# Performance work log

Measured on AMD Instinct MI355X. Metric: run time of the kernel, lower is better.

## Reference

```python
import jax, jax.numpy as jnp
import numpy as np

B, S, D, UNITS = 4, 512, 256, 128
NEG = -1e9


def setup_inputs() -> dict:
    key = jax.random.key(0)
    k1, k2, k3, k4 = jax.random.split(key, 4)
    values = jax.random.normal(k1, (B, S, D), dtype=jnp.float32)
    Wq = jax.random.normal(k2, (D, UNITS), dtype=jnp.float32) * (1.0 / np.sqrt(D))
    Wv = jax.random.normal(k3, (D, UNITS), dtype=jnp.float32) * (1.0 / np.sqrt(D))
    Vw = jax.random.normal(k4, (UNITS,), dtype=jnp.float32) * (1.0 / np.sqrt(UNITS))
    return {"values": values, "Wq": Wq, "Wv": Wv, "Vw": Vw}


def reference(values, Wq, Wv, Vw):
    # values: [B, S, D]
    query = values @ Wq            # [B, S, U]
    value = values @ Wv            # [B, S, U]
    # additive (Bahdanau) score: V . tanh(q_i + v_j) -> [B, S, S]
    feat = jnp.tanh(query[:, :, None, :] + value[:, None, :, :])  # [B,S,S,U]
    score = jnp.einsum('biju,u->bij', feat, Vw)
    seq_len = values.shape[1]
    causal = jnp.tril(jnp.ones((seq_len, seq_len), dtype=jnp.float32))  # lower-tri = visible
    score = score + (1.0 - causal)[None, :, :] * jnp.asarray(NEG, score.dtype)
    attn = jax.nn.softmax(score, axis=-1)          # [B, S, S]
    context = jnp.matmul(attn, values)             # [B, S, D]
    return context
```

## Files before the change

kernel.cpp:

```cpp
#include <hip/hip_runtime.h>
#include <hip/hip_fp16.h>

#define SEQ 512
#define DIM 256
#define UN  128
#define BSZ 2048
#define CSC 2.8853900817779268f

struct h8 { __half2 a, b, c, d; };

__global__ __launch_bounds__(256) void proj_kernel(
    const float* __restrict__ values, const float* __restrict__ Wq,
    const float* __restrict__ Wv, float* __restrict__ Qc, float* __restrict__ Vc,
    __half* __restrict__ Vf16) {
  __shared__ float vsm[4 * DIM];
  const int t = threadIdx.x;
  const int r0 = blockIdx.x * 4;
  {
    const int row = t >> 6, c4 = (t & 63) * 4;
    const float4 v = *(const float4*)(values + (r0 + row) * DIM + c4);
    *(float4*)&vsm[row * DIM + c4] = v;
    __half2* vf = (__half2*)(Vf16 + (r0 + row) * DIM + c4);
    vf[0] = __floats2half2_rn(v.x, v.y);
    vf[1] = __floats2half2_rn(v.z, v.w);
  }
  __syncthreads();
  const int half = t >> 7, u = t & 127;
  const float* __restrict__ W = half ? Wv : Wq;
  float acc[4] = {0.f, 0.f, 0.f, 0.f};
  for (int d = 0; d < DIM; d += 4) {
    const float w0 = W[(d + 0) * UN + u], w1 = W[(d + 1) * UN + u];
    const float w2 = W[(d + 2) * UN + u], w3 = W[(d + 3) * UN + u];
#pragma unroll
    for (int k = 0; k < 4; ++k) {
      const float4 v = *(const float4*)&vsm[k * DIM + d];
      acc[k] = fmaf(v.x, w0, acc[k]);
      acc[k] = fmaf(v.y, w1, acc[k]);
      acc[k] = fmaf(v.z, w2, acc[k]);
      acc[k] = fmaf(v.w, w3, acc[k]);
    }
  }
  if (!half) {
#pragma unroll
    for (int k = 0; k < 4; ++k) Qc[(r0 + k) * UN + u] = acc[k] * CSC;
  } else {
    const float4 o = make_float4(acc[0] * CSC, acc[1] * CSC, acc[2] * CSC, acc[3] * CSC);
    *(float4*)(Vc + u * BSZ + r0) = o;
  }
}

__global__ __launch_bounds__(256, 4) void attn_kernel(
    const __half* __restrict__ Vf16, const float* __restrict__ Qc,
    const float* __restrict__ Vc, const float* __restrict__ Vw,
    float* __restrict__ out) {
  __shared__ float sc[2 * SEQ];
  __shared__ float scp[2 * SEQ];
  __shared__ float part[8 * DIM];
  __shared__ float invs[2];

  const int t = threadIdx.x;
  const int b = blockIdx.x >> 8, p = blockIdx.x & 255;
  const int bS = b * SEQ;
  const int i = p;
  const int ihi = SEQ - 1 - p;
  const int jhi = ihi;

  const float* __restrict__ qlo = Qc + (bS + i) * UN;
  const float* __restrict__ qhi = Qc + (bS + ihi) * UN;

  {
    const int qd = t & 127;
    const int u0 = (t >> 7) << 6;
    const int jb = qd << 2;
    float* __restrict__ so = (t >> 7) ? scp : sc;
    const float* __restrict__ vq = Vc + bS + jb;
    if ((t & 64) == 0) {
      float h0=0.f,h1=0.f,h2=0.f,h3=0.f,l0=0.f,l1=0.f,l2=0.f,l3=0.f;
#pragma unroll 2
      for (int u = u0; u < u0 + 64; ++u) {
        const float4 vc = *(const float4*)(vq + (size_t)u * BSZ);
        const float qh = qhi[u], ql = qlo[u], w = Vw[u];
        h0 = fmaf(w, __builtin_amdgcn_rcpf(__builtin_amdgcn_exp2f(qh + vc.x) + 1.f), h0);
        h1 = fmaf(w, __builtin_amdgcn_rcpf(__builtin_amdgcn_exp2f(qh + vc.y) + 1.f), h1);
        h2 = fmaf(w, __builtin_amdgcn_rcpf(__builtin_amdgcn_exp2f(qh + vc.z) + 1.f), h2);
        h3 = fmaf(w, __builtin_amdgcn_rcpf(__builtin_amdgcn_exp2f(qh + vc.w) + 1.f), h3);
        l0 = fmaf(w, __builtin_amdgcn_rcpf(__builtin_amdgcn_exp2f(ql + vc.x) + 1.f), l0);
        l1 = fmaf(w, __builtin_amdgcn_rcpf(__builtin_amdgcn_exp2f(ql + vc.y) + 1.f), l1);
        l2 = fmaf(w, __builtin_amdgcn_rcpf(__builtin_amdgcn_exp2f(ql + vc.z) + 1.f), l2);
        l3 = fmaf(w, __builtin_amdgcn_rcpf(__builtin_amdgcn_exp2f(ql + vc.w) + 1.f), l3);
      }
      *(float4*)&so[SEQ + jb] = make_float4(h0, h1, h2, h3);
      *(float4*)&so[jb]       = make_float4(l0, l1, l2, l3);
    } else if (jb <= jhi) {
      float h0=0.f,h1=0.f,h2=0.f,h3=0.f;
#pragma unroll 4
      for (int u = u0; u < u0 + 64; ++u) {
        const float4 vc = *(const float4*)(vq + (size_t)u * BSZ);
        const float qh = qhi[u], w = Vw[u];
        h0 = fmaf(w, __builtin_amdgcn_rcpf(__builtin_amdgcn_exp2f(qh + vc.x) + 1.f), h0);
        h1 = fmaf(w, __builtin_amdgcn_rcpf(__builtin_amdgcn_exp2f(qh + vc.y) + 1.f), h1);
        h2 = fmaf(w, __builtin_amdgcn_rcpf(__builtin_amdgcn_exp2f(qh + vc.z) + 1.f), h2);
        h3 = fmaf(w, __builtin_amdgcn_rcpf(__builtin_amdgcn_exp2f(qh + vc.w) + 1.f), h3);
      }
      *(float4*)&so[SEQ + jb] = make_float4(h0, h1, h2, h3);
    }
  }
  __syncthreads();

  {
    const int w = t >> 6, l = t & 63;
    if (w < 2) {
      const int jmax = (w == 0) ? i : jhi;
      float* __restrict__ r0p = sc + w * SEQ;
      const float* __restrict__ r1p = scp + w * SEQ;
      float m = 1e30f;
      for (int j = l; j <= jmax; j += 64) m = fminf(m, r0p[j] + r1p[j]);
#pragma unroll
      for (int o = 32; o; o >>= 1) m = fminf(m, __shfl_xor(m, o));
      float sum = 0.f;
      for (int j = l; j <= jmax; j += 64) {
        const float pr = __builtin_amdgcn_exp2f((m - (r0p[j] + r1p[j])) * CSC);
        r0p[j] = pr;
        sum += pr;
      }
#pragma unroll
      for (int o = 32; o; o >>= 1) sum += __shfl_xor(sum, o);
      if (l == 0) invs[w] = __builtin_amdgcn_rcpf(sum);
    }
  }
  __syncthreads();

  {
    const int g = t >> 6, l = t & 63;
    const int jo = l >> 5, d8 = (l & 31) << 3;
    float alo[8], ahi[8];
#pragma unroll
    for (int k = 0; k < 8; ++k) { alo[k] = 0.f; ahi[k] = 0.f; }
    int j = 2 * g + jo;
    for (; j <= i; j += 8) {
      const float plo = sc[j], phi = sc[SEQ + j];
      const h8 v = *(const h8*)(Vf16 + (size_t)(bS + j) * DIM + d8);
      const float2 f0 = __half22float2(v.a), f1 = __half22float2(v.b);
      const float2 f2 = __half22float2(v.c), f3 = __half22float2(v.d);
      alo[0] = fmaf(plo, f0.x, alo[0]); alo[1] = fmaf(plo, f0.y, alo[1]);
      alo[2] = fmaf(plo, f1.x, alo[2]); alo[3] = fmaf(plo, f1.y, alo[3]);
      alo[4] = fmaf(plo, f2.x, alo[4]); alo[5] = fmaf(plo, f2.y, alo[5]);
      alo[6] = fmaf(plo, f3.x, alo[6]); alo[7] = fmaf(plo, f3.y, alo[7]);
      ahi[0] = fmaf(phi, f0.x, ahi[0]); ahi[1] = fmaf(phi, f0.y, ahi[1]);
      ahi[2] = fmaf(phi, f1.x, ahi[2]); ahi[3] = fmaf(phi, f1.y, ahi[3]);
      ahi[4] = fmaf(phi, f2.x, ahi[4]); ahi[5] = fmaf(phi, f2.y, ahi[5]);
      ahi[6] = fmaf(phi, f3.x, ahi[6]); ahi[7] = fmaf(phi, f3.y, ahi[7]);
    }
    for (; j <= jhi; j += 8) {
      const float phi = sc[SEQ + j];
      const h8 v = *(const h8*)(Vf16 + (size_t)(bS + j) * DIM + d8);
      const float2 f0 = __half22float2(v.a), f1 = __half22float2(v.b);
      const float2 f2 = __half22float2(v.c), f3 = __half22float2(v.d);
      ahi[0] = fmaf(phi, f0.x, ahi[0]); ahi[1] = fmaf(phi, f0.y, ahi[1]);
      ahi[2] = fmaf(phi, f1.x, ahi[2]); ahi[3] = fmaf(phi, f1.y, ahi[3]);
      ahi[4] = fmaf(phi, f2.x, ahi[4]); ahi[5] = fmaf(phi, f2.y, ahi[5]);
      ahi[6] = fmaf(phi, f3.x, ahi[6]); ahi[7] = fmaf(phi, f3.y, ahi[7]);
    }
#pragma unroll
    for (int k = 0; k < 8; ++k) {
      alo[k] += __shfl_xor(alo[k], 32);
      ahi[k] += __shfl_xor(ahi[k], 32);
    }
    if (jo == 0) {
      float* __restrict__ plo_ = &part[(g * 2 + 0) * DIM + d8];
      float* __restrict__ phi_ = &part[(g * 2 + 1) * DIM + d8];
      *(float4*)(plo_ + 0) = make_float4(alo[0], alo[1], alo[2], alo[3]);
      *(float4*)(plo_ + 4) = make_float4(alo[4], alo[5], alo[6], alo[7]);
      *(float4*)(phi_ + 0) = make_float4(ahi[0], ahi[1], ahi[2], ahi[3]);
      *(float4*)(phi_ + 4) = make_float4(ahi[4], ahi[5], ahi[6], ahi[7]);
    }
  }
  __syncthreads();

  {
    const float olo = (part[0 * DIM + t] + part[2 * DIM + t] +
                       part[4 * DIM + t] + part[6 * DIM + t]) * invs[0];
    const float ohi = (part[1 * DIM + t] + part[3 * DIM + t] +
                       part[5 * DIM + t] + part[7 * DIM + t]) * invs[1];
    out[(bS + i) * DIM + t] = olo;
    out[(bS + ihi) * DIM + t] = ohi;
  }
}

extern "C" void kernel_launch(void* const* d_in, const int* in_sizes, int n_in,
                              void* d_out, int out_size, void* d_ws, size_t ws_size,
                              hipStream_t stream) {
  const float* values = (const float*)d_in[0];
  const float* Wq     = (const float*)d_in[1];
  const float* Wv     = (const float*)d_in[2];
  const float* Vw     = (const float*)d_in[3];
  float* out = (float*)d_out;
  float* Qc   = (float*)d_ws;
  float* Vc   = Qc + (size_t)BSZ * UN;
  __half* Vf16 = (__half*)(Vc + (size_t)BSZ * UN);
  proj_kernel<<<dim3(BSZ / 4), 256, 0, stream>>>(values, Wq, Wv, Qc, Vc, Vf16);
  attn_kernel<<<dim3(4 * 256), 256, 0, stream>>>(Vf16, Qc, Vc, Vw, out);
}
```

Before: 118.1 us.

## Factor exp2 out of score inner loop and store value exponentials as bf16

Uses exp2(q+v)=exp2(q)*exp2(v) to precompute exponentials of the scaled query and value projections in the projection kernel. The score loop then needs only an fma and a reciprocal per element instead of an exp plus a reciprocal. The value exponentials are stored in bf16 to halve their read traffic. The score and context loops also software-prefetch the next row, at the cost of precision and overflow risk when exp2 of large projections is taken separately.

```diff
diff --git a/kernel.cpp b/kernel.cpp
--- a/kernel.cpp
+++ b/kernel.cpp
@@ -9,10 +9,19 @@
 
 struct h8 { __half2 a, b, c, d; };
 
+static __device__ __forceinline__ unsigned short f2bf(float x) {
+  unsigned u = __float_as_uint(x);
+  u += 0x7FFF + ((u >> 16) & 1);
+  return (unsigned short)(u >> 16);
+}
+static __device__ __forceinline__ float bf2f(unsigned short s) {
+  return __uint_as_float((unsigned)s << 16);
+}
+
 __global__ __launch_bounds__(256) void proj_kernel(
     const float* __restrict__ values, const float* __restrict__ Wq,
-    const float* __restrict__ Wv, float* __restrict__ Qc, float* __restrict__ Vc,
-    __half* __restrict__ Vf16) {
+    const float* __restrict__ Wv, float* __restrict__ Eq,
+    unsigned short* __restrict__ Ev, __half* __restrict__ Vf16) {
   __shared__ float vsm[4 * DIM];
   const int t = threadIdx.x;
   const int r0 = blockIdx.x * 4;
@@ -42,16 +51,21 @@
   }
   if (!half) {
 #pragma unroll
-    for (int k = 0; k < 4; ++k) Qc[(r0 + k) * UN + u] = acc[k] * CSC;
+    for (int k = 0; k < 4; ++k)
+      Eq[(r0 + k) * UN + u] = __builtin_amdgcn_exp2f(acc[k] * CSC);
   } else {
-    const float4 o = make_float4(acc[0] * CSC, acc[1] * CSC, acc[2] * CSC, acc[3] * CSC);
-    *(float4*)(Vc + u * BSZ + r0) = o;
+    ushort4 o;
+    o.x = f2bf(__builtin_amdgcn_exp2f(acc[0] * CSC));
+    o.y = f2bf(__builtin_amdgcn_exp2f(acc[1] * CSC));
+    o.z = f2bf(__builtin_amdgcn_exp2f(acc[2] * CSC));
+    o.w = f2bf(__builtin_amdgcn_exp2f(acc[3] * CSC));
+    *(ushort4*)(Ev + (size_t)u * BSZ + r0) = o;
   }
 }
 
 __global__ __launch_bounds__(256, 4) void attn_kernel(
-    const __half* __restrict__ Vf16, const float* __restrict__ Qc,
-    const float* __restrict__ Vc, const float* __restrict__ Vw,
+    const __half* __restrict__ Vf16, const float* __restrict__ Eq,
+    const unsigned short* __restrict__ Ev, const float* __restrict__ Vw,
     float* __restrict__ out) {
   __shared__ float sc[2 * SEQ];
   __shared__ float scp[2 * SEQ];
@@ -65,42 +79,46 @@
   const int ihi = SEQ - 1 - p;
   const int jhi = ihi;
 
-  const float* __restrict__ qlo = Qc + (bS + i) * UN;
-  const float* __restrict__ qhi = Qc + (bS + ihi) * UN;
-
-  {
-    const int qd = t & 127;
+  const float* __restrict__ eql = Eq + (bS + i) * UN;
+  const float* __restrict__ eqh = Eq + (bS + ihi) * UN;
+
+  {
+    const int qd = t & 127, jb = qd << 2;
     const int u0 = (t >> 7) << 6;
-    const int jb = qd << 2;
     float* __restrict__ so = (t >> 7) ? scp : sc;
-    const float* __restrict__ vq = Vc + bS + jb;
+    const unsigned short* __restrict__ evp = Ev + (size_t)u0 * BSZ + bS + jb;
     if ((t & 64) == 0) {
       float h0=0.f,h1=0.f,h2=0.f,h3=0.f,l0=0.f,l1=0.f,l2=0.f,l3=0.f;
-#pragma unroll 2
-      for (int u = u0; u < u0 + 64; ++u) {
-        const float4 vc = *(const float4*)(vq + (size_t)u * BSZ);
-        const float qh = qhi[u], ql = qlo[u], w = Vw[u];
-        h0 = fmaf(w, __builtin_amdgcn_rcpf(__builtin_amdgcn_exp2f(qh + vc.x) + 1.f), h0);
-        h1 = fmaf(w, __builtin_amdgcn_rcpf(__builtin_amdgcn_exp2f(qh + vc.y) + 1.f), h1);
-        h2 = fmaf(w, __builtin_amdgcn_rcpf(__builtin_amdgcn_exp2f(qh + vc.z) + 1.f), h2);
-        h3 = fmaf(w, __builtin_amdgcn_rcpf(__builtin_amdgcn_exp2f(qh + vc.w) + 1.f), h3);
-        l0 = fmaf(w, __builtin_amdgcn_rcpf(__builtin_amdgcn_exp2f(ql + vc.x) + 1.f), l0);
-        l1 = fmaf(w, __builtin_amdgcn_rcpf(__builtin_amdgcn_exp2f(ql + vc.y) + 1.f), l1);
-        l2 = fmaf(w, __builtin_amdgcn_rcpf(__builtin_amdgcn_exp2f(ql + vc.z) + 1.f), l2);
-        l3 = fmaf(w, __builtin_amdgcn_rcpf(__builtin_amdgcn_exp2f(ql + vc.w) + 1.f), l3);
+      ushort4 ec = *(const ushort4*)evp;
+#pragma unroll 4
+      for (int k = 0; k < 64; ++k) {
+        const ushort4 en = *(const ushort4*)(evp + (size_t)(k + 1) * BSZ);
+        const float qh = eqh[u0 + k], ql = eql[u0 + k], w = Vw[u0 + k];
+        const float e0 = bf2f(ec.x), e1 = bf2f(ec.y), e2 = bf2f(ec.z), e3 = bf2f(ec.w);
+        h0 = fmaf(w, __builtin_amdgcn_rcpf(fmaf(qh, e0, 1.f)), h0);
+        h1 = fmaf(w, __builtin_amdgcn_rcpf(fmaf(qh, e1, 1.f)), h1);
+        h2 = fmaf(w, __builtin_amdgcn_rcpf(fmaf(qh, e2, 1.f)), h2);
+        h3 = fmaf(w, __builtin_amdgcn_rcpf(fmaf(qh, e3, 1.f)), h3);
+        l0 = fmaf(w, __builtin_amdgcn_rcpf(fmaf(ql, e0, 1.f)), l0);
+        l1 = fmaf(w, __builtin_amdgcn_rcpf(fmaf(ql, e1, 1.f)), l1);
+        l2 = fmaf(w, __builtin_amdgcn_rcpf(fmaf(ql, e2, 1.f)), l2);
+        l3 = fmaf(w, __builtin_amdgcn_rcpf(fmaf(ql, e3, 1.f)), l3);
+        ec = en;
       }
       *(float4*)&so[SEQ + jb] = make_float4(h0, h1, h2, h3);
       *(float4*)&so[jb]       = make_float4(l0, l1, l2, l3);
     } else if (jb <= jhi) {
       float h0=0.f,h1=0.f,h2=0.f,h3=0.f;
+      ushort4 ec = *(const ushort4*)evp;
 #pragma unroll 4
-      for (int u = u0; u < u0 + 64; ++u) {
-        const float4 vc = *(const float4*)(vq + (size_t)u * BSZ);
-        const float qh = qhi[u], w = Vw[u];
-        h0 = fmaf(w, __builtin_amdgcn_rcpf(__builtin_amdgcn_exp2f(qh + vc.x) + 1.f), h0);
-        h1 = fmaf(w, __builtin_amdgcn_rcpf(__builtin_amdgcn_exp2f(qh + vc.y) + 1.f), h1);
-        h2 = fmaf(w, __builtin_amdgcn_rcpf(__builtin_amdgcn_exp2f(qh + vc.z) + 1.f), h2);
-        h3 = fmaf(w, __builtin_amdgcn_rcpf(__builtin_amdgcn_exp2f(qh + vc.w) + 1.f), h3);
+      for (int k = 0; k < 64; ++k) {
+        const ushort4 en = *(const ushort4*)(evp + (size_t)(k + 1) * BSZ);
+        const float qh = eqh[u0 + k], w = Vw[u0 + k];
+        h0 = fmaf(w, __builtin_amdgcn_rcpf(fmaf(qh, bf2f(ec.x), 1.f)), h0);
+        h1 = fmaf(w, __builtin_amdgcn_rcpf(fmaf(qh, bf2f(ec.y), 1.f)), h1);
+        h2 = fmaf(w, __builtin_amdgcn_rcpf(fmaf(qh, bf2f(ec.z), 1.f)), h2);
+        h3 = fmaf(w, __builtin_amdgcn_rcpf(fmaf(qh, bf2f(ec.w), 1.f)), h3);
+        ec = en;
       }
       *(float4*)&so[SEQ + jb] = make_float4(h0, h1, h2, h3);
     }
@@ -137,11 +155,13 @@
 #pragma unroll
     for (int k = 0; k < 8; ++k) { alo[k] = 0.f; ahi[k] = 0.f; }
     int j = 2 * g + jo;
+    h8 vc = *(const h8*)(Vf16 + (size_t)(bS + j) * DIM + d8);
     for (; j <= i; j += 8) {
+      const int jn = (j + 8 <= jhi) ? j + 8 : jhi;
+      const h8 vn = *(const h8*)(Vf16 + (size_t)(bS + jn) * DIM + d8);
       const float plo = sc[j], phi = sc[SEQ + j];
-      const h8 v = *(const h8*)(Vf16 + (size_t)(bS + j) * DIM + d8);
-      const float2 f0 = __half22float2(v.a), f1 = __half22float2(v.b);
-      const float2 f2 = __half22float2(v.c), f3 = __half22float2(v.d);
+      const float2 f0 = __half22float2(vc.a), f1 = __half22float2(vc.b);
+      const float2 f2 = __half22float2(vc.c), f3 = __half22float2(vc.d);
       alo[0] = fmaf(plo, f0.x, alo[0]); alo[1] = fmaf(plo, f0.y, alo[1]);
       alo[2] = fmaf(plo, f1.x, alo[2]); alo[3] = fmaf(plo, f1.y, alo[3]);
       alo[4] = fmaf(plo, f2.x, alo[4]); alo[5] = fmaf(plo, f2.y, alo[5]);
@@ -150,16 +170,19 @@
       ahi[2] = fmaf(phi, f1.x, ahi[2]); ahi[3] = fmaf(phi, f1.y, ahi[3]);
       ahi[4] = fmaf(phi, f2.x, ahi[4]); ahi[5] = fmaf(phi, f2.y, ahi[5]);
       ahi[6] = fmaf(phi, f3.x, ahi[6]); ahi[7] = fmaf(phi, f3.y, ahi[7]);
+      vc = vn;
     }
     for (; j <= jhi; j += 8) {
+      const int jn = (j + 8 <= jhi) ? j + 8 : jhi;
+      const h8 vn = *(const h8*)(Vf16 + (size_t)(bS + jn) * DIM + d8);
       const float phi = sc[SEQ + j];
-      const h8 v = *(const h8*)(Vf16 + (size_t)(bS + j) * DIM + d8);
-      const float2 f0 = __half22float2(v.a), f1 = __half22float2(v.b);
-      const float2 f2 = __half22float2(v.c), f3 = __half22float2(v.d);
+      const float2 f0 = __half22float2(vc.a), f1 = __half22float2(vc.b);
+      const float2 f2 = __half22float2(vc.c), f3 = __half22float2(vc.d);
       ahi[0] = fmaf(phi, f0.x, ahi[0]); ahi[1] = fmaf(phi, f0.y, ahi[1]);
       ahi[2] = fmaf(phi, f1.x, ahi[2]); ahi[3] = fmaf(phi, f1.y, ahi[3]);
       ahi[4] = fmaf(phi, f2.x, ahi[4]); ahi[5] = fmaf(phi, f2.y, ahi[5]);
       ahi[6] = fmaf(phi, f3.x, ahi[6]); ahi[7] = fmaf(phi, f3.y, ahi[7]);
+      vc = vn;
     }
 #pragma unroll
     for (int k = 0; k < 8; ++k) {
@@ -195,9 +218,9 @@
   const float* Wv     = (const float*)d_in[2];
   const float* Vw     = (const float*)d_in[3];
   float* out = (float*)d_out;
-  float* Qc   = (float*)d_ws;
-  float* Vc   = Qc + (size_t)BSZ * UN;
-  __half* Vf16 = (__half*)(Vc + (size_t)BSZ * UN);
-  proj_kernel<<<dim3(BSZ / 4), 256, 0, stream>>>(values, Wq, Wv, Qc, Vc, Vf16);
-  attn_kernel<<<dim3(4 * 256), 256, 0, stream>>>(Vf16, Qc, Vc, Vw, out);
-}
+  float* Eq = (float*)d_ws;
+  unsigned short* Ev = (unsigned short*)(Eq + (size_t)BSZ * UN);
+  __half* Vf16 = (__half*)(Ev + (size_t)UN * BSZ);
+  proj_kernel<<<dim3(BSZ / 4), 256, 0, stream>>>(values, Wq, Wv, Eq, Ev, Vf16);
+  attn_kernel<<<dim3(4 * 256), 256, 0, stream>>>(Vf16, Eq, Ev, Vw, out);
+}
```

New measurement: 105.4 us. 1.12x faster.
